# Performance work log

Hardware: AMD Instinct MI355X
Metric: run time of the kernel (lower is better)

The kernel has to match this reference:

```python
import jax, jax.numpy as jnp
import numpy as np

H, DR, DN = 16, 64, 64
HD = DR + DN  # 128
EPS = 1e-6


def _ln(t):
    m = t.mean(-1, keepdims=True)
    v = ((t - m) ** 2).mean(-1, keepdims=True)
    return (t - m) / jnp.sqrt(v + EPS)


def _rms(t, w):
    return t * jax.lax.rsqrt((t * t).mean(-1, keepdims=True) + EPS) * w


def _rot(t, fcs):
    # t: [b,s,h,DR]; fcs: [s, DR//2, 2] (cos,sin); complex multiply on pairs
    b, s, h, d = t.shape
    tr = t.reshape(b, s, h, d // 2, 2)
    x0, x1 = tr[..., 0], tr[..., 1]
    cos = fcs[None, :, None, :, 0]
    sin = fcs[None, :, None, :, 1]
    o0 = x0 * cos - x1 * sin
    o1 = x0 * sin + x1 * cos
    return jnp.stack([o0, o1], axis=-1).reshape(b, s, h, d)


def setup_inputs() -> dict:
    key = jax.random.key(0)
    ks = jax.random.split(key, 12)
    B, SX, SY, D = 1, 2048, 512, 2048
    s = 0.02
    pos_x = jnp.arange(SX, dtype=jnp.float32)
    pos_y = jnp.arange(SY, dtype=jnp.float32)
    inv = 1.0 / (10000.0 ** (jnp.arange(0, DR, 2, dtype=jnp.float32) / DR))  # [32]
    ang_x = pos_x[:, None] * inv[None, :]
    ang_y = pos_y[:, None] * inv[None, :]
    return {
        "x": jax.random.normal(ks[0], (B, SX, D), jnp.float32),
        "y": jax.random.normal(ks[1], (B, SY, D), jnp.float32),
        "mod": jax.random.normal(ks[2], (B, D), jnp.float32),
        "freqs_x": jnp.stack([jnp.cos(ang_x), jnp.sin(ang_x)], -1),
        "freqs_y": jnp.stack([jnp.cos(ang_y), jnp.sin(ang_y)], -1),
        "mask_x": jnp.ones((B, SX), bool),
        "mask_y": jnp.ones((B, SY), bool),
        "Wqkv_x": jax.random.normal(ks[3], (HD * H * 3, D), jnp.float32) * s,
        "bqkv_x": jnp.zeros((HD * H * 3,), jnp.float32),
        "Wqkv_y": jax.random.normal(ks[4], (HD * H * 3, D), jnp.float32) * s,
        "bqkv_y": jnp.zeros((HD * H * 3,), jnp.float32),
        "Wout": jax.random.normal(ks[5], (D, HD * H), jnp.float32) * s,
        "bout": jnp.zeros((D,), jnp.float32),
        "wq": jnp.ones((HD,), jnp.float32),
        "wk": jnp.ones((HD,), jnp.float32),
        "Wmod_q": jax.random.normal(ks[6], (D * 3, D), jnp.float32) * s,
        "bmod_q": jnp.zeros((D * 3,), jnp.float32),
        "Wmod_kv": jax.random.normal(ks[7], (D * 3, D), jnp.float32) * s,
        "bmod_kv": jnp.zeros((D * 3,), jnp.float32),
    }


def reference(x, y, mod, freqs_x, freqs_y, mask_x, mask_y, Wqkv_x, bqkv_x,
              Wqkv_y, bqkv_y, Wout, bout, wq, wk, Wmod_q, bmod_q, Wmod_kv, bmod_kv):
    b, sx, D = x.shape
    sy = y.shape[1]
    sz = sx + sy
    x_res, y_res = x, y
    xn = _ln(x)
    yn = _ln(y)
    # modulation from mod vector [b, D] -> [b, 1, 3D]
    mq = mod[:, None, :] @ Wmod_q.T + bmod_q
    bias_x, scale_x, gate_x = jnp.split(mq, 3, axis=-1)
    mkv = mod[:, None, :] @ Wmod_kv.T + bmod_kv
    bias_y, scale_y, gate_y = jnp.split(mkv, 3, axis=-1)
    xm = (1.0 + scale_x) * xn + bias_x
    ym = (1.0 + scale_y) * yn + bias_y
    qx, kx, vx = jnp.split(xm @ Wqkv_x.T + bqkv_x, 3, axis=-1)
    qy, ky, vy = jnp.split(ym @ Wqkv_y.T + bqkv_y, 3, axis=-1)
    q = jnp.concatenate([qx, qy], 1).reshape(b, sz, H, HD)
    k = jnp.concatenate([kx, ky], 1).reshape(b, sz, H, HD)
    v = jnp.concatenate([vx, vy], 1).reshape(b, sz, H, HD)
    q = _rms(q, wq)
    k = _rms(k, wk)
    q_rope, q_nope = q[..., :DR], q[..., DR:]
    k_rope, k_nope = k[..., :DR], k[..., DR:]
    fxx = jnp.concatenate([freqs_x, jnp.zeros_like(freqs_y)], 0)
    fyy = jnp.concatenate([jnp.zeros_like(freqs_x), freqs_y], 0)
    qf = jnp.concatenate([_rot(q_rope, fxx), _rot(q_rope, fyy), q_nope], -1)
    kf = jnp.concatenate([_rot(k_rope, fxx), _rot(k_rope, fyy), k_nope], -1)
    d_attn = 2 * DR + DN  # 192
    scale = 1.0 / jnp.sqrt(jnp.float32(d_attn))
    scores = jnp.einsum('bshd,bthd->bhst', qf, kf) * scale
    mask = jnp.concatenate([mask_x, mask_y], 1)  # [b, sz] bool, key-side
    scores = jnp.where(mask[:, None, None, :], scores, -jnp.inf)
    attn = jax.nn.softmax(scores, axis=-1)
    z = jnp.einsum('bhst,bthd->bshd', attn, v).reshape(b, sz, H * HD)
    z = z @ Wout.T + bout
    xo = z[:, :sx] * gate_x + x_res
    yo = z[:, sx:] * gate_y + y_res
    return jnp.concatenate([xo, yo], axis=1)  # [b, sz, D]
```

## Files before the change

kernel.cpp:

```cpp
#include <hip/hip_runtime.h>
#include <math.h>

#define H_    16
#define DR_   64
#define HD_   128
#define D_    2048
#define SX_   2048
#define SY_   512
#define SZ_   2560
#define NQKV_ 6144
#define EPS_  1e-6f
#define ATTN_SCALE_L2E 0.10412035f
#define NS_   4
#define SPL_  (SZ_ / NS_)
#define QT_   (SZ_ / 128)

typedef __attribute__((ext_vector_type(8)))  short short8;
typedef __attribute__((ext_vector_type(16))) float f32x16;

__device__ __forceinline__ unsigned short f2bf(float f) {
    unsigned u = __builtin_bit_cast(unsigned, f);
    u += 0x7FFF + ((u >> 16) & 1);
    return (unsigned short)(u >> 16);
}
__device__ __forceinline__ unsigned pack2(float a, float b) {
    return (unsigned)f2bf(a) | ((unsigned)f2bf(b) << 16);
}
__device__ __forceinline__ float bf2f_lo(unsigned u) {
    return __builtin_bit_cast(float, u << 16);
}
__device__ __forceinline__ float bf2f_hi(unsigned u) {
    return __builtin_bit_cast(float, u & 0xffff0000u);
}

__device__ __forceinline__ float fexp2(float x) {
    return __builtin_amdgcn_exp2f(x);
}

__device__ __forceinline__ unsigned cvtpk_bf16(float lo, float hi) {
    unsigned r;
    asm volatile("v_cvt_pk_bf16_f32 %0, %1, %2" : "=v"(r) : "v"(lo), "v"(hi));
    return r;
}

__device__ __forceinline__ void gload16(const unsigned short* g, unsigned short* l) {
    __builtin_amdgcn_global_load_lds(
        (const __attribute__((address_space(1))) unsigned*)g,
        (__attribute__((address_space(3))) unsigned*)l, 16, 0, 0);
}

__device__ __forceinline__ int xcd_swz(int hw, int nwg) {
    return (hw & 7) * (nwg >> 3) + (hw >> 3);
}

__device__ __forceinline__ short8 mkfrag(const float* p) {
    unsigned a01 = cvtpk_bf16(p[0], p[1]);
    unsigned a23 = cvtpk_bf16(p[2], p[3]);
    unsigned a45 = cvtpk_bf16(p[4], p[5]);
    unsigned a67 = cvtpk_bf16(p[6], p[7]);
    asm volatile("v_permlane32_swap_b32 %0, %1" : "+v"(a01), "+v"(a45));
    asm volatile("v_permlane32_swap_b32 %0, %1" : "+v"(a23), "+v"(a67));
    union { unsigned u[4]; short8 s; } r;
    r.u[0] = a01; r.u[1] = a23; r.u[2] = a45; r.u[3] = a67;
    return r.s;
}

__global__ __launch_bounds__(256) void cvt_all_kernel(
    const float* __restrict__ s1, const float* __restrict__ s2, const float* __restrict__ s3,
    unsigned short* __restrict__ dst, int n1, int n2, int n3)
{
    int i = (blockIdx.x * 256 + threadIdx.x) * 8;
    if (i >= n1 + n2 + n3) return;
    const float* src;
    if (i < n1)            src = s1 + i;
    else if (i < n1 + n2)  src = s2 + (i - n1);
    else                   src = s3 + (i - n1 - n2);
    float4 a = *(const float4*)(src);
    float4 b = *(const float4*)(src + 4);
    uint4 pk;
    pk.x = pack2(a.x, a.y); pk.y = pack2(a.z, a.w);
    pk.z = pack2(b.x, b.y); pk.w = pack2(b.z, b.w);
    *(uint4*)(dst + i) = pk;
}

__global__ __launch_bounds__(256) void mod_gemv_kernel(
    const float* __restrict__ mod,
    const float* __restrict__ Wq, const float* __restrict__ bq,
    const float* __restrict__ Wkv, const float* __restrict__ bkv,
    float* __restrict__ mq, float* __restrict__ mkv)
{
    int t = threadIdx.x;
    int row = blockIdx.x * 4 + (t >> 6);
    int lane = t & 63;
    const float* W; const float* b; float* out; int r;
    if (row < NQKV_) { W = Wq;  b = bq;  out = mq;  r = row; }
    else             { W = Wkv; b = bkv; out = mkv; r = row - NQKV_; }
    const float* wr = W + (size_t)r * D_;
    float s = 0.f;
    for (int k = lane; k < D_; k += 64) s += wr[k] * mod[k];
#pragma unroll
    for (int m = 32; m >= 1; m >>= 1) s += __shfl_xor(s, m);
    if (lane == 0) out[r] = s + b[r];
}

__global__ __launch_bounds__(256) void ln_mod_kernel(
    const float* __restrict__ x, const float* __restrict__ y,
    const float* __restrict__ mq, const float* __restrict__ mkv,
    unsigned short* __restrict__ xm)
{
    __shared__ float red[8];
    int s = blockIdx.x, t = threadIdx.x;
    const float* src; const float* mv;
    if (s < SX_) { src = x + (size_t)s * D_;          mv = mq; }
    else         { src = y + (size_t)(s - SX_) * D_;  mv = mkv; }
    float a[8];
    *(float4*)&a[0] = *(const float4*)(src + t * 8);
    *(float4*)&a[4] = *(const float4*)(src + t * 8 + 4);
    float sum = 0.f, ssq = 0.f;
#pragma unroll
    for (int i = 0; i < 8; ++i) { sum += a[i]; ssq += a[i] * a[i]; }
#pragma unroll
    for (int m = 32; m >= 1; m >>= 1) { sum += __shfl_xor(sum, m); ssq += __shfl_xor(ssq, m); }
    if ((t & 63) == 0) { red[t >> 6] = sum; red[4 + (t >> 6)] = ssq; }
    __syncthreads();
    float tot  = red[0] + red[1] + red[2] + red[3];
    float totq = red[4] + red[5] + red[6] + red[7];
    float mean = tot * (1.f / (float)D_);
    float var  = totq * (1.f / (float)D_) - mean * mean;
    float inv  = rsqrtf(var + EPS_);
    float o[8];
#pragma unroll
    for (int i = 0; i < 8; ++i) {
        int c = t * 8 + i;
        float v = (a[i] - mean) * inv;
        o[i] = (1.f + mv[D_ + c]) * v + mv[c];
    }
    uint4 pk;
    pk.x = pack2(o[0], o[1]); pk.y = pack2(o[2], o[3]);
    pk.z = pack2(o[4], o[5]); pk.w = pack2(o[6], o[7]);
    *(uint4*)(xm + (size_t)s * D_ + t * 8) = pk;
}

__global__ __launch_bounds__(512, 2) void gemm8_bf16_kernel(
    const unsigned short* __restrict__ A,
    const unsigned short* __restrict__ Wx, const float* __restrict__ bx,
    const unsigned short* __restrict__ Wy, const float* __restrict__ by,
    unsigned short* __restrict__ C, int N)
{
    __shared__ __align__(16) unsigned short As[2][256 * 64];
    __shared__ __align__(16) unsigned short Bs[2][256 * 64];
    int m0 = blockIdx.y * 256, n0 = blockIdx.x * 256;
    const unsigned short* W = (m0 < SX_) ? Wx : Wy;
    const float* bb = (m0 < SX_) ? bx : by;
    int t = threadIdx.x;
    int wv = t >> 6, lane = t & 63, l31 = lane & 31, g = lane >> 5;
    int wr = wv >> 2, wc = wv & 3;
    int off[4];
#pragma unroll
    for (int i = 0; i < 4; ++i) {
        int c = i * 512 + t, r = c >> 3, sl = c & 7;
        off[i] = r * D_ + ((sl ^ (r & 7)) * 8);
    }
    const unsigned short* gA = A + (size_t)m0 * D_;
    const unsigned short* gW = W + (size_t)n0 * D_;
    int dstw = wv * 512;
    f32x16 acc[4][2];
#pragma unroll
    for (int i = 0; i < 4; ++i)
#pragma unroll
        for (int j = 0; j < 2; ++j)
#pragma unroll
            for (int r = 0; r < 16; ++r) acc[i][j][r] = 0.f;
    int arow = wr * 128 + l31;
    int brow = wc * 64 + l31;
    int s7 = l31 & 7;

#pragma unroll
    for (int i = 0; i < 4; ++i) gload16(gA + off[i], &As[0][i * 4096 + dstw]);
#pragma unroll
    for (int i = 0; i < 4; ++i) gload16(gW + off[i], &Bs[0][i * 4096 + dstw]);

    const int NT = D_ / 64;
    for (int kt = 0; kt < NT; ++kt) {
        int cur = kt & 1;
        asm volatile("s_waitcnt vmcnt(0)" ::: "memory");
        __builtin_amdgcn_s_barrier();
        if (kt + 1 < NT) {
            int nb = cur ^ 1, k1 = (kt + 1) * 64;
#pragma unroll
            for (int i = 0; i < 4; ++i) gload16(gA + k1 + off[i], &As[nb][i * 4096 + dstw]);
#pragma unroll
            for (int i = 0; i < 4; ++i) gload16(gW + k1 + off[i], &Bs[nb][i * 4096 + dstw]);
        }
#pragma unroll
        for (int ks = 0; ks < 4; ++ks) {
            int sx = ((ks * 2 + g) ^ s7) * 8;
            short8 af[4], bf[2];
#pragma unroll
            for (int i = 0; i < 4; ++i)
                af[i] = *(const short8*)&As[cur][(arow + i * 32) * 64 + sx];
#pragma unroll
            for (int j = 0; j < 2; ++j)
                bf[j] = *(const short8*)&Bs[cur][(brow + j * 32) * 64 + sx];
#pragma unroll
            for (int i = 0; i < 4; ++i)
#pragma unroll
                for (int j = 0; j < 2; ++j)
                    acc[i][j] = __builtin_amdgcn_mfma_f32_32x32x16_bf16(bf[j], af[i], acc[i][j], 0, 0, 0);
        }
    }

#pragma unroll
    for (int i = 0; i < 4; ++i) {
        int row = m0 + wr * 128 + i * 32 + l31;
#pragma unroll
        for (int j = 0; j < 2; ++j)
#pragma unroll
            for (int q = 0; q < 4; ++q) {
                int n = n0 + wc * 64 + j * 32 + q * 8 + 4 * g;
                float o0 = acc[i][j][q * 4 + 0] + bb[n + 0];
                float o1 = acc[i][j][q * 4 + 1] + bb[n + 1];
                float o2 = acc[i][j][q * 4 + 2] + bb[n + 2];
                float o3 = acc[i][j][q * 4 + 3] + bb[n + 3];
                *(uint2*)(C + (size_t)row * N + n) = make_uint2(pack2(o0, o1), pack2(o2, o3));
            }
    }
}

__global__ __launch_bounds__(256) void gemm_bf16_kernel(
    const unsigned short* __restrict__ A,
    const unsigned short* __restrict__ Wx, const float* __restrict__ bx,
    const unsigned short* __restrict__ Wy, const float* __restrict__ by,
    void* __restrict__ Cout, int N,
    const float* __restrict__ gx, const float* __restrict__ gy,
    const float* __restrict__ rx, const float* __restrict__ ry,
    int mode)
{
    __shared__ __align__(16) unsigned short As[2][128 * 32];
    __shared__ __align__(16) unsigned short Bs[2][128 * 32];
    int m0 = blockIdx.y * 128, n0 = blockIdx.x * 128;
    const unsigned short* W = (m0 < SX_) ? Wx : Wy;
    const float* bb = (m0 < SX_) ? bx : by;
    int t = threadIdx.x;
    int wv = t >> 6, lane = t & 63, l31 = lane & 31, g = lane >> 5;
    int wr = wv >> 1, wc = wv & 1;
    int srow = t >> 2, ssl = t & 3;
    const unsigned short* gA = A + (size_t)(m0 + srow) * D_ + ((ssl ^ ((srow >> 1) & 3)) * 8);
    const unsigned short* gW = W + (size_t)(n0 + srow) * D_ + ((ssl ^ ((srow >> 1) & 3)) * 8);
    f32x16 acc[2][2];
#pragma unroll
    for (int i = 0; i < 2; ++i)
#pragma unroll
        for (int j = 0; j < 2; ++j)
#pragma unroll
            for (int r = 0; r < 16; ++r) acc[i][j][r] = 0.f;
    int arow = wr * 64 + l31;
    int wrow = wc * 64 + l31;
    int a3 = (arow >> 1) & 3, w3 = (wrow >> 1) & 3;

    gload16(gA,            &As[0][wv * 512]);
    gload16(gA + 64 * D_,  &As[0][2048 + wv * 512]);
    gload16(gW,            &Bs[0][wv * 512]);
    gload16(gW + 64 * D_,  &Bs[0][2048 + wv * 512]);
    __syncthreads();

    for (int k0 = 0; k0 < D_; k0 += 32) {
        int cur = (k0 >> 5) & 1;
        if (k0 + 32 < D_) {
            int nb = cur ^ 1;
            gload16(gA + k0 + 32,           &As[nb][wv * 512]);
            gload16(gA + 64 * D_ + k0 + 32, &As[nb][2048 + wv * 512]);
            gload16(gW + k0 + 32,           &Bs[nb][wv * 512]);
            gload16(gW + 64 * D_ + k0 + 32, &Bs[nb][2048 + wv * 512]);
        }
#pragma unroll
        for (int kk = 0; kk < 2; ++kk) {
            int slot = kk * 2 + g;
            short8 af[2], wf[2];
#pragma unroll
            for (int i = 0; i < 2; ++i) {
                af[i] = *(const short8*)&As[cur][(arow + i * 32) * 32 + ((slot ^ a3) * 8)];
                wf[i] = *(const short8*)&Bs[cur][(wrow + i * 32) * 32 + ((slot ^ w3) * 8)];
            }
#pragma unroll
            for (int i = 0; i < 2; ++i)
#pragma unroll
                for (int j = 0; j < 2; ++j)
                    acc[i][j] = __builtin_amdgcn_mfma_f32_32x32x16_bf16(wf[j], af[i], acc[i][j], 0, 0, 0);
        }
        __syncthreads();
    }

#pragma unroll
    for (int i = 0; i < 2; ++i) {
        int row = m0 + wr * 64 + i * 32 + l31;
        if (mode == 0) {
            unsigned short* C = (unsigned short*)Cout;
#pragma unroll
            for (int j = 0; j < 2; ++j)
#pragma unroll
                for (int q = 0; q < 4; ++q) {
                    int n = n0 + wc * 64 + j * 32 + q * 8 + 4 * g;
                    float o0 = acc[i][j][q * 4 + 0] + bb[n + 0];
                    float o1 = acc[i][j][q * 4 + 1] + bb[n + 1];
                    float o2 = acc[i][j][q * 4 + 2] + bb[n + 2];
                    float o3 = acc[i][j][q * 4 + 3] + bb[n + 3];
                    *(uint2*)(C + (size_t)row * N + n) = make_uint2(pack2(o0, o1), pack2(o2, o3));
                }
        } else {
            float* C = (float*)Cout;
            const float* gt = (row < SX_) ? gx : gy;
            const float* rr = (row < SX_) ? rx + (size_t)row * N : ry + (size_t)(row - SX_) * N;
#pragma unroll
            for (int j = 0; j < 2; ++j)
#pragma unroll
                for (int q = 0; q < 4; ++q) {
                    int n = n0 + wc * 64 + j * 32 + q * 8 + 4 * g;
                    float4 o;
                    o.x = (acc[i][j][q * 4 + 0] + bb[n + 0]) * gt[n + 0] + rr[n + 0];
                    o.y = (acc[i][j][q * 4 + 1] + bb[n + 1]) * gt[n + 1] + rr[n + 1];
                    o.z = (acc[i][j][q * 4 + 2] + bb[n + 2]) * gt[n + 2] + rr[n + 2];
                    o.w = (acc[i][j][q * 4 + 3] + bb[n + 3]) * gt[n + 3] + rr[n + 3];
                    *(float4*)(C + (size_t)row * N + n) = o;
                }
        }
    }
}

__global__ __launch_bounds__(256) void qkv_transform_kernel(
    const unsigned short* __restrict__ qkv,
    const float* __restrict__ fx, const float* __restrict__ fy,
    const float* __restrict__ wq, const float* __restrict__ wk,
    unsigned short* __restrict__ qh, unsigned short* __restrict__ kh)
{
    int t = threadIdx.x;
    int gid = blockIdx.x * 4 + (t >> 6);
    int lane = t & 63;
    int s = gid >> 4;
    int h = gid & 15;
    const unsigned short* base = qkv + (size_t)s * NQKV_ + h * HD_;
    int d = lane * 2;
    unsigned qu = *(const unsigned*)(base + d);
    unsigned ku = *(const unsigned*)(base + 2048 + d);
    float qx = bf2f_lo(qu), qy = bf2f_hi(qu);
    float kx = bf2f_lo(ku), ky = bf2f_hi(ku);
    float sq = qx * qx + qy * qy;
    float sk = kx * kx + ky * ky;
#pragma unroll
    for (int m = 32; m >= 1; m >>= 1) { sq += __shfl_xor(sq, m); sk += __shfl_xor(sk, m); }
    float qs = rsqrtf(sq * (1.f / 128.f) + EPS_) * ATTN_SCALE_L2E;
    float ks = rsqrtf(sk * (1.f / 128.f) + EPS_);
    float q0 = qx * qs * wq[d], q1 = qy * qs * wq[d + 1];
    float k0 = kx * ks * wk[d], k1 = ky * ks * wk[d + 1];
    if (lane < 32) {
        const float* f = (s < SX_) ? fx + (size_t)s * DR_ + d
                                   : fy + (size_t)(s - SX_) * DR_ + d;
        float cs = f[0], sn = f[1];
        float o0 = q0 * cs - q1 * sn, o1 = q0 * sn + q1 * cs;
        q0 = o0; q1 = o1;
        o0 = k0 * cs - k1 * sn; o1 = k0 * sn + k1 * cs;
        k0 = o0; k1 = o1;
    }
    size_t off = ((size_t)h * SZ_ + s) * HD_ + d;
    *(unsigned*)(qh + off) = pack2(q0, q1);
    *(unsigned*)(kh + off) = pack2(k0, k1);
}

__global__ __launch_bounds__(256) void vtrans_kernel(
    const unsigned short* __restrict__ qkvb, unsigned short* __restrict__ vt)
{
    __shared__ __align__(16) unsigned short T[64][72];
    int h = blockIdx.z, d0 = blockIdx.y * 64, s0 = blockIdx.x * 64;
    int t = threadIdx.x;
    int r = t >> 2, c = (t & 3) * 16;
    const unsigned short* src = qkvb + (size_t)(s0 + r) * NQKV_ + 4096 + h * HD_ + d0 + c;
    *(short8*)&T[r][c]     = *(const short8*)(src);
    *(short8*)&T[r][c + 8] = *(const short8*)(src + 8);
    __syncthreads();
    unsigned short o16[16];
#pragma unroll
    for (int i = 0; i < 16; ++i) o16[i] = T[c + i][r];
    unsigned short* dst = vt + ((size_t)h * HD_ + d0 + r) * SZ_ + s0 + c;
    *(short8*)dst       = *(short8*)&o16[0];
    *(short8*)(dst + 8) = *(short8*)&o16[8];
}

__global__ __launch_bounds__(256) void attn_mfma_kernel(
    const unsigned short* __restrict__ qh, const unsigned short* __restrict__ kh,
    const unsigned short* __restrict__ vt,
    unsigned short* __restrict__ Opart, float* __restrict__ mpart, float* __restrict__ lpart)
{
    __shared__ __align__(16) short Ks[2][64 * 128];
    __shared__ __align__(16) short Vs[2][128 * 64];
    int hw = (blockIdx.z * gridDim.y + blockIdx.y) * gridDim.x + blockIdx.x;
    int lg = xcd_swz(hw, QT_ * H_ * NS_);
    int qt    = lg % QT_;
    int hs    = lg / QT_;
    int h     = hs % H_;
    int split = hs / H_;
    int t = threadIdx.x;
    int wv = t >> 6, lane = t & 63;
    int l31 = lane & 31, g = lane >> 5;
    int bq = qt * 128 + wv * 32;
    const unsigned short* kbase = kh + (size_t)h * SZ_ * HD_;
    const unsigned short* vbase = vt + (size_t)h * HD_ * SZ_;

    int koff[4], voff[4];
#pragma unroll
    for (int i = 0; i < 4; ++i) {
        int idx = i * 256 + t;
        int r = idx >> 4, sl = idx & 15;
        koff[i] = r * HD_ + (((sl & 8) | ((sl ^ (r & 7)) & 7)) * 8);
        int r2 = idx >> 3, sl2 = idx & 7;
        voff[i] = r2 * SZ_ + ((sl2 ^ (r2 & 7)) * 8);
    }
    int ldsOff = wv * 512;

    short8 qf[8];
    {
        const unsigned short* qb = qh + ((size_t)h * SZ_ + bq + l31) * HD_ + g * 8;
#pragma unroll
        for (int s = 0; s < 8; ++s) qf[s] = *(const short8*)(qb + s * 16);
    }

    f32x16 o[4];
#pragma unroll
    for (int db = 0; db < 4; ++db)
#pragma unroll
        for (int r = 0; r < 16; ++r) o[db][r] = 0.f;
    float mreg = -INFINITY, lreg = 0.f;
    bool qY = (bq >= SX_);
    int sw7 = l31 & 7;
    int ts0 = split * SPL_;
    const int NT = SPL_ / 64;

#pragma unroll
    for (int i = 0; i < 4; ++i)
        gload16(kbase + (size_t)ts0 * HD_ + koff[i], (unsigned short*)&Ks[0][0] + i * 2048 + ldsOff);
#pragma unroll
    for (int i = 0; i < 4; ++i)
        gload16(vbase + ts0 + voff[i], (unsigned short*)&Vs[0][0] + i * 2048 + ldsOff);
    __syncthreads();

    for (int it = 0; it < NT; ++it) {
        int t0 = ts0 + it * 64;
        int cur = it & 1;
        if (it + 1 < NT) {
            int nb = cur ^ 1;
            const unsigned short* kn = kbase + (size_t)(t0 + 64) * HD_;
            const unsigned short* vn = vbase + (t0 + 64);
#pragma unroll
            for (int i = 0; i < 4; ++i)
                gload16(kn + koff[i], (unsigned short*)&Ks[nb][0] + i * 2048 + ldsOff);
#pragma unroll
            for (int i = 0; i < 4; ++i)
                gload16(vn + voff[i], (unsigned short*)&Vs[nb][0] + i * 2048 + ldsOff);
        }

        bool same = (qY == (t0 >= SX_));
        f32x16 sc0, sc1;
#pragma unroll
        for (int r = 0; r < 16; ++r) { sc0[r] = 0.f; sc1[r] = 0.f; }
        const short* Krow0 = &Ks[cur][0] + l31 * 128;
        const short* Krow1 = &Ks[cur][0] + (l31 + 32) * 128;
        __builtin_amdgcn_s_setprio(1);
#pragma unroll
        for (int s = 4; s < 8; ++s) {
            int slot = 2 * s + g;
            int sl = (slot & 8) | ((slot ^ sw7) & 7);
            sc0 = __builtin_amdgcn_mfma_f32_32x32x16_bf16(*(const short8*)(Krow0 + sl * 8), qf[s], sc0, 0, 0, 0);
            sc1 = __builtin_amdgcn_mfma_f32_32x32x16_bf16(*(const short8*)(Krow1 + sl * 8), qf[s], sc1, 0, 0, 0);
        }
        if (same) {
#pragma unroll
            for (int s = 0; s < 4; ++s) {
                int slot = 2 * s + g;
                int sl = (slot & 8) | ((slot ^ sw7) & 7);
                sc0 = __builtin_amdgcn_mfma_f32_32x32x16_bf16(*(const short8*)(Krow0 + sl * 8), qf[s], sc0, 0, 0, 0);
                sc1 = __builtin_amdgcn_mfma_f32_32x32x16_bf16(*(const short8*)(Krow1 + sl * 8), qf[s], sc1, 0, 0, 0);
            }
        }
        __builtin_amdgcn_s_setprio(0);

        float pm = -INFINITY;
#pragma unroll
        for (int r = 0; r < 16; ++r) pm = fmaxf(pm, fmaxf(sc0[r], sc1[r]));
        pm = fmaxf(pm, __shfl_xor(pm, 32));
        float mnew = fmaxf(mreg, pm);
        float corr = fexp2(mreg - mnew);
        mreg = mnew;
        float pp0[16], pp1[16]; float rs = 0.f;
#pragma unroll
        for (int r = 0; r < 16; ++r) {
            pp0[r] = fexp2(sc0[r] - mnew);
            pp1[r] = fexp2(sc1[r] - mnew);
            rs += pp0[r] + pp1[r];
        }
        rs += __shfl_xor(rs, 32);
        lreg = lreg * corr + rs;
#pragma unroll
        for (int db = 0; db < 4; ++db)
#pragma unroll
            for (int r = 0; r < 16; ++r) o[db][r] *= corr;

        short8 pa0 = mkfrag(&pp0[0]), pa1 = mkfrag(&pp0[8]);
        short8 pa2 = mkfrag(&pp1[0]), pa3 = mkfrag(&pp1[8]);
        const short* Vb = &Vs[cur][0];
        __builtin_amdgcn_s_setprio(1);
#pragma unroll
        for (int ks = 0; ks < 4; ++ks) {
            short8 pf = (ks == 0) ? pa0 : (ks == 1) ? pa1 : (ks == 2) ? pa2 : pa3;
#pragma unroll
            for (int db = 0; db < 4; ++db) {
                int row = db * 32 + l31;
                int sl = (2 * ks + g) ^ (l31 & 7);
                const short8 vf = *(const short8*)(Vb + row * 64 + sl * 8);
                o[db] = __builtin_amdgcn_mfma_f32_32x32x16_bf16(vf, pf, o[db], 0, 0, 0);
            }
        }
        __builtin_amdgcn_s_setprio(0);
        __syncthreads();
    }

    int basep = ((split * QT_ + qt) * H_ + h) * 128 + wv * 32 + l31;
    unsigned short* op = Opart + (size_t)basep * 128;
#pragma unroll
    for (int db = 0; db < 4; ++db)
#pragma unroll
        for (int q = 0; q < 4; ++q) {
            int d = db * 32 + q * 8 + 4 * g;
            *(uint2*)(op + d) = make_uint2(
                pack2(o[db][q * 4 + 0], o[db][q * 4 + 1]),
                pack2(o[db][q * 4 + 2], o[db][q * 4 + 3]));
        }
    if (g == 0) { mpart[basep] = mreg; lpart[basep] = lreg; }
}

__global__ __launch_bounds__(256) void attn_combine_kernel(
    const unsigned short* __restrict__ Opart,
    const float* __restrict__ mpart, const float* __restrict__ lpart,
    unsigned short* __restrict__ z)
{
    int t = threadIdx.x;
    int gid = blockIdx.x * 4 + (t >> 6);
    int lane = t & 63;
    int h = gid & 15;
    int r = gid >> 4;
    int qtile = r >> 7, qi = r & 127;
    int pidx[NS_];
    float m[NS_];
    float mx = -INFINITY;
#pragma unroll
    for (int s = 0; s < NS_; ++s) {
        pidx[s] = ((s * QT_ + qtile) * H_ + h) * 128 + qi;
        m[s] = mpart[pidx[s]];
        mx = fmaxf(mx, m[s]);
    }
    float L = 0.f;
    float w[NS_];
#pragma unroll
    for (int s = 0; s < NS_; ++s) {
        w[s] = fexp2(m[s] - mx);
        L += w[s] * lpart[pidx[s]];
    }
    float invL = 1.f / L;
    int d = lane * 2;
    float a0 = 0.f, a1 = 0.f;
#pragma unroll
    for (int s = 0; s < NS_; ++s) {
        unsigned u = *(const unsigned*)(Opart + (size_t)pidx[s] * 128 + d);
        a0 += w[s] * bf2f_lo(u);
        a1 += w[s] * bf2f_hi(u);
    }
    *(unsigned*)(z + (size_t)r * D_ + h * HD_ + d) = pack2(a0 * invL, a1 * invL);
}

extern "C" void kernel_launch(void* const* d_in, const int* in_sizes, int n_in,
                              void* d_out, int out_size, void* d_ws, size_t ws_size,
                              hipStream_t stream) {
    const float* x    = (const float*)d_in[0];
    const float* y    = (const float*)d_in[1];
    const float* mod  = (const float*)d_in[2];
    const float* fx   = (const float*)d_in[3];
    const float* fy   = (const float*)d_in[4];
    const float* Wqx  = (const float*)d_in[7];
    const float* bqx  = (const float*)d_in[8];
    const float* Wqy  = (const float*)d_in[9];
    const float* bqy  = (const float*)d_in[10];
    const float* Wout = (const float*)d_in[11];
    const float* bout = (const float*)d_in[12];
    const float* wq   = (const float*)d_in[13];
    const float* wk   = (const float*)d_in[14];
    const float* Wmq  = (const float*)d_in[15];
    const float* bmq  = (const float*)d_in[16];
    const float* Wmk  = (const float*)d_in[17];
    const float* bmk  = (const float*)d_in[18];

    float* mq   = (float*)d_ws;
    float* mkv  = mq + NQKV_;
    unsigned short* xm   = (unsigned short*)(mkv + NQKV_);
    unsigned short* qkvb = xm + (size_t)SZ_ * D_;
    unsigned short* qh   = qkvb + (size_t)SZ_ * NQKV_;
    unsigned short* kh   = qh + (size_t)H_ * SZ_ * HD_;
    unsigned short* vh   = kh + (size_t)H_ * SZ_ * HD_;
    unsigned short* vt   = vh + (size_t)H_ * SZ_ * HD_;
    unsigned short* wqxb = vt + (size_t)H_ * SZ_ * HD_;
    unsigned short* wqyb = wqxb + (size_t)NQKV_ * D_;
    unsigned short* wob  = wqyb + (size_t)NQKV_ * D_;
    unsigned short* z    = xm;
    unsigned short* Opart = wqxb;
    float* mpart = (float*)qkvb;
    float* lpart = mpart + NS_ * QT_ * H_ * 128;
    float* out  = (float*)d_out;

    const int n1 = NQKV_ * D_, n3 = D_ * D_;
    hipLaunchKernelGGL(cvt_all_kernel, dim3((2 * n1 + n3) / 2048), dim3(256), 0, stream,
                       Wqx, Wqy, Wout, wqxb, n1, n1, n3);
    hipLaunchKernelGGL(mod_gemv_kernel, dim3(2 * NQKV_ / 4), dim3(256), 0, stream,
                       mod, Wmq, bmq, Wmk, bmk, mq, mkv);
    hipLaunchKernelGGL(ln_mod_kernel, dim3(SZ_), dim3(256), 0, stream,
                       x, y, mq, mkv, xm);
    hipLaunchKernelGGL(gemm8_bf16_kernel, dim3(NQKV_ / 256, SZ_ / 256), dim3(512), 0, stream,
                       xm, wqxb, bqx, wqyb, bqy, qkvb, NQKV_);
    hipLaunchKernelGGL(qkv_transform_kernel, dim3(SZ_ * H_ / 4), dim3(256), 0, stream,
                       qkvb, fx, fy, wq, wk, qh, kh);
    hipLaunchKernelGGL(vtrans_kernel, dim3(SZ_ / 64, HD_ / 64, H_), dim3(256), 0, stream,
                       qkvb, vt);
    hipLaunchKernelGGL(attn_mfma_kernel, dim3(QT_, H_, NS_), dim3(256), 0, stream,
                       qh, kh, vt, Opart, mpart, lpart);
    hipLaunchKernelGGL(attn_combine_kernel, dim3(SZ_ * H_ / 4), dim3(256), 0, stream,
                       Opart, mpart, lpart, z);
    hipLaunchKernelGGL(gemm_bf16_kernel, dim3(D_ / 128, SZ_ / 128), dim3(256), 0, stream,
                       z, wob, bout, wob, bout, (void*)out, D_,
                       mq + 2 * D_, mkv + 2 * D_, x, y, 1);
}
```

Before: 317.1 us.

## Fuse QKV weight fp32-to-bf16 conversion into the QKV GEMM load path

The separate conversion pass over both QKV weight matrices is removed. The GEMM now loads fp32 weights into registers, packs them to bf16 and stores them to shared memory itself, with an extra LDS wait and barrier per k-tile. This avoids writing and re-reading the bf16 weight copies. In exchange the GEMM reads twice the weight bytes, re-converts each weight tile for every M-block that uses it, and adds synchronisation plus register pressure to the main loop.

After: 320.0 us. Within noise of the previous version (+0.9%).

```diff
diff --git a/kernel.cpp b/kernel.cpp
--- a/kernel.cpp
+++ b/kernel.cpp
@@ -143,26 +143,32 @@
 
 __global__ __launch_bounds__(512, 2) void gemm8_bf16_kernel(
     const unsigned short* __restrict__ A,
-    const unsigned short* __restrict__ Wx, const float* __restrict__ bx,
-    const unsigned short* __restrict__ Wy, const float* __restrict__ by,
+    const float* __restrict__ Wfx, const float* __restrict__ bx,
+    const float* __restrict__ Wfy, const float* __restrict__ by,
     unsigned short* __restrict__ C, int N)
 {
     __shared__ __align__(16) unsigned short As[2][256 * 64];
     __shared__ __align__(16) unsigned short Bs[2][256 * 64];
     int m0 = blockIdx.y * 256, n0 = blockIdx.x * 256;
-    const unsigned short* W = (m0 < SX_) ? Wx : Wy;
+    const float* Wf = (m0 < SX_) ? Wfx : Wfy;
     const float* bb = (m0 < SX_) ? bx : by;
     int t = threadIdx.x;
     int wv = t >> 6, lane = t & 63, l31 = lane & 31, g = lane >> 5;
     int wr = wv >> 2, wc = wv & 3;
-    int off[4];
+    int offA[4];
 #pragma unroll
     for (int i = 0; i < 4; ++i) {
         int c = i * 512 + t, r = c >> 3, sl = c & 7;
-        off[i] = r * D_ + ((sl ^ (r & 7)) * 8);
+        offA[i] = r * D_ + ((sl ^ (r & 7)) * 8);
+    }
+    int wr_[4], ws_[4];
+#pragma unroll
+    for (int i = 0; i < 4; ++i) {
+        int c = i * 512 + t;
+        wr_[i] = c >> 3; ws_[i] = c & 7;
     }
     const unsigned short* gA = A + (size_t)m0 * D_;
-    const unsigned short* gW = W + (size_t)n0 * D_;
+    const float* gWf = Wf + (size_t)n0 * D_;
     int dstw = wv * 512;
     f32x16 acc[4][2];
 #pragma unroll
@@ -176,22 +182,42 @@
     int s7 = l31 & 7;
 
 #pragma unroll
-    for (int i = 0; i < 4; ++i) gload16(gA + off[i], &As[0][i * 4096 + dstw]);
-#pragma unroll
-    for (int i = 0; i < 4; ++i) gload16(gW + off[i], &Bs[0][i * 4096 + dstw]);
+    for (int i = 0; i < 4; ++i) gload16(gA + offA[i], &As[0][i * 4096 + dstw]);
+    float4 wlo[4], whi[4];
+#pragma unroll
+    for (int i = 0; i < 4; ++i) {
+        const float* p = gWf + (size_t)wr_[i] * D_ + ws_[i] * 8;
+        wlo[i] = *(const float4*)p;
+        whi[i] = *(const float4*)(p + 4);
+    }
 
     const int NT = D_ / 64;
     for (int kt = 0; kt < NT; ++kt) {
         int cur = kt & 1;
         asm volatile("s_waitcnt vmcnt(0)" ::: "memory");
         __builtin_amdgcn_s_barrier();
+#pragma unroll
+        for (int i = 0; i < 4; ++i) {
+            uint4 pk;
+            pk.x = pack2(wlo[i].x, wlo[i].y);
+            pk.y = pack2(wlo[i].z, wlo[i].w);
+            pk.z = pack2(whi[i].x, whi[i].y);
+            pk.w = pack2(whi[i].z, whi[i].w);
+            *(uint4*)&Bs[cur][wr_[i] * 64 + ((ws_[i] ^ (wr_[i] & 7)) * 8)] = pk;
+        }
         if (kt + 1 < NT) {
             int nb = cur ^ 1, k1 = (kt + 1) * 64;
 #pragma unroll
-            for (int i = 0; i < 4; ++i) gload16(gA + k1 + off[i], &As[nb][i * 4096 + dstw]);
-#pragma unroll
-            for (int i = 0; i < 4; ++i) gload16(gW + k1 + off[i], &Bs[nb][i * 4096 + dstw]);
-        }
+            for (int i = 0; i < 4; ++i) gload16(gA + k1 + offA[i], &As[nb][i * 4096 + dstw]);
+#pragma unroll
+            for (int i = 0; i < 4; ++i) {
+                const float* p = gWf + (size_t)wr_[i] * D_ + k1 + ws_[i] * 8;
+                wlo[i] = *(const float4*)p;
+                whi[i] = *(const float4*)(p + 4);
+            }
+        }
+        asm volatile("s_waitcnt lgkmcnt(0)" ::: "memory");
+        __builtin_amdgcn_s_barrier();
 #pragma unroll
         for (int ks = 0; ks < 4; ++ks) {
             int sx = ((ks * 2 + g) ^ s7) * 8;
@@ -613,15 +639,15 @@
     float* lpart = mpart + NS_ * QT_ * H_ * 128;
     float* out  = (float*)d_out;
 
-    const int n1 = NQKV_ * D_, n3 = D_ * D_;
-    hipLaunchKernelGGL(cvt_all_kernel, dim3((2 * n1 + n3) / 2048), dim3(256), 0, stream,
-                       Wqx, Wqy, Wout, wqxb, n1, n1, n3);
+    const int n3 = D_ * D_;
+    hipLaunchKernelGGL(cvt_all_kernel, dim3(n3 / 2048), dim3(256), 0, stream,
+                       Wout, Wout, Wout, wob, 0, 0, n3);
     hipLaunchKernelGGL(mod_gemv_kernel, dim3(2 * NQKV_ / 4), dim3(256), 0, stream,
                        mod, Wmq, bmq, Wmk, bmk, mq, mkv);
     hipLaunchKernelGGL(ln_mod_kernel, dim3(SZ_), dim3(256), 0, stream,
                        x, y, mq, mkv, xm);
     hipLaunchKernelGGL(gemm8_bf16_kernel, dim3(NQKV_ / 256, SZ_ / 256), dim3(512), 0, stream,
-                       xm, wqxb, bqx, wqyb, bqy, qkvb, NQKV_);
+                       xm, Wqx, bqx, Wqy, bqy, qkvb, NQKV_);
     hipLaunchKernelGGL(qkv_transform_kernel, dim3(SZ_ * H_ / 4), dim3(256), 0, stream,
                        qkvb, fx, fy, wq, wk, qh, kh);
     hipLaunchKernelGGL(vtrans_kernel, dim3(SZ_ / 64, HD_ / 64, H_), dim3(256), 0, stream,
```
